# Optimization experiments

Hardware: AMD Instinct MI355X
Metric: run time of the kernel (lower is better)

Reference implementation:

```python
import jax, jax.numpy as jnp
import numpy as np

N = 5000
NFEAT = 512
NHID = 64
NHEADS = 8
NCLASS = 40
ALPHA = 0.2  # leaky relu slope
NEG_INF = -9e15


def setup_inputs() -> dict:
    key = jax.random.key(0)
    ks = jax.random.split(key, 12)
    x = jax.random.normal(ks[0], (N, NFEAT), dtype=jnp.float32)
    # binary adjacency, ~32 avg degree, with self loops
    adj = (jax.random.uniform(ks[1], (N, N)) < (32.0 / N)).astype(jnp.float32)
    adj = jnp.maximum(adj, jnp.eye(N, dtype=jnp.float32))
    s = 1.0 / np.sqrt(NFEAT)
    W_h = jax.random.uniform(ks[2], (NHEADS, NFEAT, NHID), minval=-s, maxval=s, dtype=jnp.float32)
    a_h = jax.random.uniform(ks[3], (NHEADS, 2 * NHID), minval=-s, maxval=s, dtype=jnp.float32)
    s2 = 1.0 / np.sqrt(NHID * NHEADS)
    W_o = jax.random.uniform(ks[4], (NHID * NHEADS, NHID), minval=-s2, maxval=s2, dtype=jnp.float32)
    a_o = jax.random.uniform(ks[5], (2 * NHID,), minval=-s2, maxval=s2, dtype=jnp.float32)
    s3 = 1.0 / np.sqrt(NHID)
    fc1_w = jax.random.uniform(ks[6], (NHID, 200), minval=-s3, maxval=s3, dtype=jnp.float32)
    fc1_b = jax.random.uniform(ks[7], (200,), minval=-s3, maxval=s3, dtype=jnp.float32)
    s4 = 1.0 / np.sqrt(200)
    fc2_w = jax.random.uniform(ks[8], (200, NCLASS), minval=-s4, maxval=s4, dtype=jnp.float32)
    fc2_b = jax.random.uniform(ks[9], (NCLASS,), minval=-s4, maxval=s4, dtype=jnp.float32)
    return {"x": x, "adj": adj, "W_h": W_h, "a_h": a_h, "W_o": W_o, "a_o": a_o,
            "fc1_w": fc1_w, "fc1_b": fc1_b, "fc2_w": fc2_w, "fc2_b": fc2_b}


def _masked_attention(e, adj):
    # e: [..., N, N]; mask where adj == 0, then row softmax
    e = jnp.where(adj > 0, e, NEG_INF)
    return jax.nn.softmax(e, axis=-1)


def reference(x, adj, W_h, a_h, W_o, a_o, fc1_w, fc1_b, fc2_w, fc2_b):
    # ---- multi-head GAT layer (concat=True), eval mode (dropout off) ----
    Wh = jnp.einsum('nf,hfo->hno', x, W_h)                 # [H, N, nhid]
    f1 = jnp.einsum('hno,ho->hn', Wh, a_h[:, :NHID])       # [H, N]
    f2 = jnp.einsum('hno,ho->hn', Wh, a_h[:, NHID:])       # [H, N]
    e = jax.nn.leaky_relu(f1[:, :, None] + f2[:, None, :], ALPHA)  # [H, N, N]
    att = _masked_attention(e, adj[None, :, :])
    h = jnp.einsum('hnm,hmo->hno', att, Wh)                # [H, N, nhid]
    h1 = jax.nn.elu(h).transpose(1, 0, 2).reshape(N, NHEADS * NHID)  # concat heads

    # ---- output GAT layer (concat=False) ----
    Wh2 = h1 @ W_o                                         # [N, nhid]
    g1 = Wh2 @ a_o[:NHID]                                  # [N]
    g2 = Wh2 @ a_o[NHID:]                                  # [N]
    e2 = jax.nn.leaky_relu(g1[:, None] + g2[None, :], ALPHA)
    att2 = _masked_attention(e2, adj)
    h2 = att2 @ Wh2                                        # [N, nhid]

    # ---- MLP head ----
    h3 = jax.nn.elu(h2 @ fc1_w + fc1_b)
    return h3 @ fc2_w + fc2_b                              # [N, nclass]
```

## Files before the change

kernel.cpp:

```cpp
#include <hip/hip_runtime.h>

typedef unsigned short u16;
typedef unsigned int u32;
typedef unsigned long long u64;
typedef __bf16 bf16_t;
typedef __bf16 bf16x8 __attribute__((ext_vector_type(8)));
typedef float f32x4 __attribute__((ext_vector_type(4)));
typedef u32 u32x4 __attribute__((ext_vector_type(4)));

#define NN 5000
#define NF 512
#define NH 64
#define HEADS 8
#define NCLS 40
#define CAP 128
#define LRELU 0.2f
#define BMW 80

#define CVT_BIG 320
#define CVT_GRID (CVT_BIG + 8)
#define BM_BLKS 1250
#define G1_BLKS (79 * HEADS)

__device__ __forceinline__ bool adj_is_bf16(const void* adj) {
    return ((*(const u32*)adj) & 0xFFFFu) != 0u;
}
__device__ __forceinline__ u16 rne_bf16(float f) {
    u32 u = __float_as_uint(f);
    u += 0x7FFFu + ((u >> 16) & 1u);
    return (u16)(u >> 16);
}
__device__ __forceinline__ float up_bf16(u16 h) {
    return __uint_as_float((u32)h << 16);
}
__device__ __forceinline__ u32x4 ntload4(const void* p, int idx) {
    return __builtin_nontemporal_load(((const u32x4*)p) + idx);
}

__global__ __launch_bounds__(256) void cvt(const void* __restrict__ x, const void* __restrict__ W_h,
                                           const void* __restrict__ adj,
                                           const void* a_h, const void* W_o, const void* a_o,
                                           const void* f1w, const void* f1b,
                                           const void* f2w, const void* f2b,
                                           u16* __restrict__ xc, u16* __restrict__ whc,
                                           float* a_hc, float* W_oc, float* a_oc,
                                           float* f1wc, float* f1bc, float* f2wc, float* f2bc) {
    const bool isb = adj_is_bf16(adj);
    const int b = blockIdx.x;
    if (b < CVT_BIG) {
        const int X4 = NN * NF / 4;
        const int T4 = X4 + HEADS * NF * NH / 4;
        for (int i = b * 256 + threadIdx.x; i < T4; i += CVT_BIG * 256) {
            if (i < X4) {
                ushort4 o;
                if (isb) {
                    o = ((const ushort4*)x)[i];
                } else {
                    u32x4 vv = ntload4(x, i);
                    o.x = rne_bf16(__uint_as_float(vv[0])); o.y = rne_bf16(__uint_as_float(vv[1]));
                    o.z = rne_bf16(__uint_as_float(vv[2])); o.w = rne_bf16(__uint_as_float(vv[3]));
                }
                ((ushort4*)xc)[i] = o;
            } else {
                const int iw = i - X4;
                u16 q[4];
                if (isb) {
                    ushort4 vv = ((const ushort4*)W_h)[iw];
                    q[0] = vv.x; q[1] = vv.y; q[2] = vv.z; q[3] = vv.w;
                } else {
                    u32x4 vv = ntload4(W_h, iw);
                    q[0] = rne_bf16(__uint_as_float(vv[0])); q[1] = rne_bf16(__uint_as_float(vv[1]));
                    q[2] = rne_bf16(__uint_as_float(vv[2])); q[3] = rne_bf16(__uint_as_float(vv[3]));
                }
                const int e0 = iw * 4;
                const int h = e0 >> 15;
                const int rem = e0 & 32767;
                const int f = rem >> 6, o0 = rem & 63;
                const int base = (h * 16 + (f >> 5)) * 2048 + ((f >> 3) & 3) * 128 + (f & 7);
                #pragma unroll
                for (int k = 0; k < 4; ++k) {
                    const int o = o0 + k;
                    whc[base + (o >> 4) * 512 + (o & 15) * 8] = q[k];
                }
            }
        }
    } else {
        const int s0 = HEADS * 2 * NH, s1 = HEADS * NH * NH, s2 = 2 * NH,
                  s3 = NH * 200, s4 = 200, s5 = 200 * NCLS, s6 = NCLS;
        const int total = s0 + s1 + s2 + s3 + s4 + s5 + s6;
        for (int i = (b - CVT_BIG) * 256 + threadIdx.x; i < total; i += 8 * 256) {
            const void* src; float* dst; int off = i;
            if (off < s0) { src = a_h; dst = a_hc; }
            else if ((off -= s0) < s1) { src = W_o;  dst = W_oc; }
            else if ((off -= s1) < s2) { src = a_o;  dst = a_oc; }
            else if ((off -= s2) < s3) { src = f1w;  dst = f1wc; }
            else if ((off -= s3) < s4) { src = f1b;  dst = f1bc; }
            else if ((off -= s4) < s5) { src = f2w;  dst = f2wc; }
            else { off -= s5;           src = f2b;  dst = f2bc; }
            dst[off] = isb ? up_bf16(((const u16*)src)[off]) : ((const float*)src)[off];
        }
    }
}

__global__ __launch_bounds__(256) void gemm1_f(const bf16_t* __restrict__ x,
                                               const bf16_t* __restrict__ Wf,
                                               const float* __restrict__ a_h,
                                               const void* __restrict__ adj,
                                               u64* __restrict__ bm,
                                               float* __restrict__ Wh,
                                               float* __restrict__ f1,
                                               float* __restrict__ f2) {
    const int lane = threadIdx.x & 63;
    const int wid  = threadIdx.x >> 6;
    const int b = blockIdx.x;

    if (b >= G1_BLKS) {
        const bool isb = adj_is_bf16(adj);
        const int r = (b - G1_BLKS) * 4 + wid;
        u64* bmrow = bm + (size_t)r * BMW;
        if (!isb) {
            const float* row = (const float*)adj + (size_t)r * NN;
            #pragma unroll
            for (int pass = 0; pass < 2; ++pass) {
                u32x4 v[10];
                #pragma unroll
                for (int k = 0; k < 10; ++k) {
                    int c = (pass * 10 + k) * 64 + lane;
                    v[k] = (c < 1250) ? ntload4(row, c) : (u32x4){0u, 0u, 0u, 0u};
                }
                #pragma unroll
                for (int k = 0; k < 10; ++k) {
                    int i = pass * 10 + k;
                    #pragma unroll
                    for (int j = 0; j < 4; ++j) {
                        u64 m = __ballot(v[k][j] != 0u);
                        if (lane == j) bmrow[i * 4 + j] = m;
                    }
                }
            }
        } else {
            const u16* row = (const u16*)adj + (size_t)r * NN;
            u32x4 v[10];
            #pragma unroll
            for (int k = 0; k < 10; ++k) {
                int c = k * 64 + lane;
                v[k] = (c < 625) ? ntload4(row, c) : (u32x4){0u, 0u, 0u, 0u};
            }
            #pragma unroll
            for (int k = 0; k < 10; ++k) {
                #pragma unroll
                for (int j = 0; j < 4; ++j) {
                    u64 mlo = __ballot((v[k][j] & 0xFFFFu) != 0u);
                    u64 mhi = __ballot((v[k][j] >> 16) != 0u);
                    if (lane == 2 * j)     bmrow[k * 8 + 2 * j]     = mlo;
                    if (lane == 2 * j + 1) bmrow[k * 8 + 2 * j + 1] = mhi;
                }
            }
        }
        return;
    }

    const int rg = b % 79;
    const int h  = b / 79;
    const int quad = lane >> 4;
    const int lr   = lane & 15;
    const int kq   = quad * 8;
    const int nCol = wid * 16 + lr;
    __shared__ float f1s[4][64], f2s[4][64];

    const bf16_t* Bf = Wf + (size_t)h * (16 * 2048) + threadIdx.x * 8;
    bf16x8 bfrag[16];
    #pragma unroll
    for (int s = 0; s < 16; ++s) bfrag[s] = *(const bf16x8*)(Bf + s * 2048);

    const float a1c = a_h[h * 128 + nCol];
    const float a2c = a_h[h * 128 + NH + nCol];

    for (int t = 0; t < 4; ++t) {
        const int rb = rg * 64 + t * 16;
        int row  = rb + lr;
        int rowc = row < NN ? row : NN - 1;
        const bf16_t* xp = x + (size_t)rowc * NF + kq;
        f32x4 acc = {0.f, 0.f, 0.f, 0.f};
        #pragma unroll
        for (int s = 0; s < 16; ++s) {
            bf16x8 a = *(const bf16x8*)(xp + s * 32);
            acc = __builtin_amdgcn_mfma_f32_16x16x32_bf16(a, bfrag[s], acc, 0, 0, 0);
        }
        #pragma unroll
        for (int r = 0; r < 4; ++r) {
            int gr = rb + quad * 4 + r;
            if (gr < NN) Wh[(size_t)gr * (HEADS * NH) + h * NH + nCol] = acc[r];
            float p1 = acc[r] * a1c, p2 = acc[r] * a2c;
            #pragma unroll
            for (int o = 8; o; o >>= 1) { p1 += __shfl_xor(p1, o); p2 += __shfl_xor(p2, o); }
            if (lr == 0) { f1s[wid][t * 16 + quad * 4 + r] = p1; f2s[wid][t * 16 + quad * 4 + r] = p2; }
        }
    }
    __syncthreads();
    if (wid == 0) {
        int gr = rg * 64 + lane;
        if (gr < NN) {
            f1[h * NN + gr] = f1s[0][lane] + f1s[1][lane] + f1s[2][lane] + f1s[3][lane];
            f2[h * NN + gr] = f2s[0][lane] + f2s[1][lane] + f2s[2][lane] + f2s[3][lane];
        }
    }
}

__global__ __launch_bounds__(256) void agg1f(const void* __restrict__ adj,
                                             const u64* __restrict__ bm,
                                             const float* __restrict__ Wh,
                                             const float* __restrict__ f1,
                                             const float* __restrict__ f2,
                                             int* __restrict__ nbr, int* __restrict__ deg,
                                             float* __restrict__ h1) {
    const bool isb = adj_is_bf16(adj);
    const int lane = threadIdx.x & 63;
    const int wid  = threadIdx.x >> 6;
    const int n = blockIdx.x;
    __shared__ int s_nbr[CAP];
    __shared__ int s_dall;
    __shared__ float s_p0[4][CAP], s_p1[4][CAP];

    if (wid == 0) {
        const u64* bmrow = bm + (size_t)n * BMW;
        int base = 0;
        #pragma unroll
        for (int r2 = 0; r2 < 2; ++r2) {
            int w = r2 * 64 + lane;
            u64 mw = (w < BMW) ? bmrow[w] : 0ull;
            int pc = __popcll(mw);
            int scan = pc;
            #pragma unroll
            for (int o = 1; o < 64; o <<= 1) {
                int t = __shfl_up(scan, o);
                if (lane >= o) scan += t;
            }
            int off = base + scan - pc;
            while (mw) {
                int bb = __ffsll(mw) - 1;
                mw &= mw - 1;
                int elem;
                if (!isb) elem = ((w >> 2) * 64 + bb) * 4 + (w & 3);
                else      elem = ((w >> 3) * 64 + bb) * 8 + (w & 7);
                if (off < CAP) s_nbr[off] = elem;
                ++off;
            }
            base += __shfl(scan, 63);
        }
        if (lane == 0) s_dall = base < CAP ? base : CAP;
    }
    __syncthreads();
    const int dall = s_dall;
    for (int i = threadIdx.x; i < dall; i += 256) nbr[(size_t)n * CAP + i] = s_nbr[i];
    if (threadIdx.x == 0) deg[n] = dall;

    const int ha = wid, hb = wid + 4;
    const int nb0 = (lane < dall) ? s_nbr[lane] : 0;
    const int nb1 = (lane + 64 < dall) ? s_nbr[lane + 64] : 0;
    const float f10 = f1[ha * NN + n], f11 = f1[hb * NN + n];
    const float* f2ha = f2 + (size_t)ha * NN;
    const float* f2hb = f2 + (size_t)hb * NN;

    float e00 = -INFINITY, e01 = -INFINITY, e10 = -INFINITY, e11 = -INFINITY;
    if (lane < dall) {
        float a = f10 + f2ha[nb0]; e00 = a > 0.f ? a : LRELU * a;
        float b = f11 + f2hb[nb0]; e10 = b > 0.f ? b : LRELU * b;
    }
    if (lane + 64 < dall) {
        float a = f10 + f2ha[nb1]; e01 = a > 0.f ? a : LRELU * a;
        float b = f11 + f2hb[nb1]; e11 = b > 0.f ? b : LRELU * b;
    }
    float mx0 = fmaxf(e00, e01), mx1 = fmaxf(e10, e11);
    #pragma unroll
    for (int o = 32; o; o >>= 1) {
        mx0 = fmaxf(mx0, __shfl_xor(mx0, o));
        mx1 = fmaxf(mx1, __shfl_xor(mx1, o));
    }
    float p00 = lane < dall ? expf(e00 - mx0) : 0.f;
    float p01 = lane + 64 < dall ? expf(e01 - mx0) : 0.f;
    float p10 = lane < dall ? expf(e10 - mx1) : 0.f;
    float p11 = lane + 64 < dall ? expf(e11 - mx1) : 0.f;
    float sm0 = p00 + p01, sm1 = p10 + p11;
    #pragma unroll
    for (int o = 32; o; o >>= 1) { sm0 += __shfl_xor(sm0, o); sm1 += __shfl_xor(sm1, o); }

    const float i0 = 1.f / sm0, i1 = 1.f / sm1;
    s_p0[wid][lane] = p00 * i0; s_p0[wid][lane + 64] = p01 * i0;
    s_p1[wid][lane] = p10 * i1; s_p1[wid][lane + 64] = p11 * i1;

    float A0 = 0.f, A1 = 0.f, A2 = 0.f, A3 = 0.f;
    float B0 = 0.f, B1 = 0.f, B2 = 0.f, B3 = 0.f;
    const float* W0 = Wh + ha * NH + lane;
    const float* W1 = Wh + hb * NH + lane;
    int j = 0;
    for (; j + 8 <= dall; j += 8) {
        #pragma unroll
        for (int u = 0; u < 8; ++u) {
            float a0 = s_p0[wid][j + u];
            float a1 = s_p1[wid][j + u];
            size_t base = (size_t)s_nbr[j + u] * (HEADS * NH);
            float w0 = W0[base], w1 = W1[base];
            if ((u & 3) == 0)      { A0 += a0 * w0; B0 += a1 * w1; }
            else if ((u & 3) == 1) { A1 += a0 * w0; B1 += a1 * w1; }
            else if ((u & 3) == 2) { A2 += a0 * w0; B2 += a1 * w1; }
            else                   { A3 += a0 * w0; B3 += a1 * w1; }
        }
    }
    for (; j < dall; ++j) {
        float a0 = s_p0[wid][j], a1 = s_p1[wid][j];
        size_t base = (size_t)s_nbr[j] * (HEADS * NH);
        A0 += a0 * W0[base]; B0 += a1 * W1[base];
    }
    float hv0 = A0 + A1 + A2 + A3;
    float hv1 = B0 + B1 + B2 + B3;
    hv0 = hv0 > 0.f ? hv0 : expf(hv0) - 1.f;
    hv1 = hv1 > 0.f ? hv1 : expf(hv1) - 1.f;
    h1[(size_t)n * (HEADS * NH) + ha * NH + lane] = hv0;
    h1[(size_t)n * (HEADS * NH) + hb * NH + lane] = hv1;
}

__global__ __launch_bounds__(256) void gemm2_4(const float* __restrict__ h1,
                                               const float* __restrict__ W_o,
                                               const float* __restrict__ a_o,
                                               float* __restrict__ Wh2,
                                               float* __restrict__ g1,
                                               float* __restrict__ g2) {
    const int t = threadIdx.x;
    const int n0 = blockIdx.x * 4;
    __shared__ float sh[4 * 512];
    __shared__ float ps[4][4][64];
    const float4* src = (const float4*)(h1 + (size_t)n0 * 512);
    ((float4*)sh)[t]       = src[t];
    ((float4*)sh)[t + 256] = src[t + 256];
    __syncthreads();
    const int o = t & 63, part = t >> 6;
    float a0 = 0.f, a1 = 0.f, a2 = 0.f, a3 = 0.f;
    const float* wo = W_o + part * 128 * 64 + o;
    const float* s0 = sh + part * 128;
    #pragma unroll 4
    for (int f = 0; f < 128; ++f) {
        float w = wo[f * 64];
        a0 += s0[f] * w; a1 += s0[512 + f] * w; a2 += s0[1024 + f] * w; a3 += s0[1536 + f] * w;
    }
    ps[part][0][o] = a0; ps[part][1][o] = a1; ps[part][2][o] = a2; ps[part][3][o] = a3;
    __syncthreads();
    const int nd = t >> 6;
    float w2 = ps[0][nd][o] + ps[1][nd][o] + ps[2][nd][o] + ps[3][nd][o];
    Wh2[(size_t)(n0 + nd) * 64 + o] = w2;
    float p1 = w2 * a_o[o], p2 = w2 * a_o[64 + o];
    #pragma unroll
    for (int s = 32; s; s >>= 1) { p1 += __shfl_xor(p1, s); p2 += __shfl_xor(p2, s); }
    if (o == 0) { g1[n0 + nd] = p1; g2[n0 + nd] = p2; }
}

__global__ __launch_bounds__(256) void agg2_mlp(const float* __restrict__ Wh2,
                                                const float* __restrict__ g1,
                                                const float* __restrict__ g2,
                                                const int* __restrict__ nbr,
                                                const int* __restrict__ deg,
                                                const float* __restrict__ fc1_w,
                                                const float* __restrict__ fc1_b,
                                                const float* __restrict__ fc2_w,
                                                const float* __restrict__ fc2_b,
                                                float* __restrict__ out) {
    const int lane = threadIdx.x & 63;
    const int wid  = threadIdx.x >> 6;
    const int t = threadIdx.x;
    const int n0 = blockIdx.x * 4;
    const int n = n0 + wid;
    __shared__ float s_alpha[4][CAP];
    __shared__ int   s_nbr[4][CAP];
    __shared__ float s_h2[4][NH];
    __shared__ float s_h3[4][200];
    __shared__ float ps2[2][4][NCLS];
    const int d = deg[n];
    const int* nb = nbr + (size_t)n * CAP;
    const float gn = g1[n];

    float mx = -INFINITY;
    for (int j = lane; j < d; j += 64) {
        int m = nb[j];
        s_nbr[wid][j] = m;
        float e = gn + g2[m];
        e = e > 0.f ? e : LRELU * e;
        s_alpha[wid][j] = e;
        mx = fmaxf(mx, e);
    }
    #pragma unroll
    for (int o = 32; o; o >>= 1) mx = fmaxf(mx, __shfl_xor(mx, o));
    float sm = 0.f;
    for (int j = lane; j < d; j += 64) {
        float p = expf(s_alpha[wid][j] - mx);
        s_alpha[wid][j] = p;
        sm += p;
    }
    #pragma unroll
    for (int o = 32; o; o >>= 1) sm += __shfl_xor(sm, o);

    float acc0 = 0.f, acc1 = 0.f, acc2 = 0.f, acc3 = 0.f;
    int j = 0;
    for (; j + 4 <= d; j += 4) {
        acc0 += s_alpha[wid][j]     * Wh2[(size_t)s_nbr[wid][j]     * NH + lane];
        acc1 += s_alpha[wid][j + 1] * Wh2[(size_t)s_nbr[wid][j + 1] * NH + lane];
        acc2 += s_alpha[wid][j + 2] * Wh2[(size_t)s_nbr[wid][j + 2] * NH + lane];
        acc3 += s_alpha[wid][j + 3] * Wh2[(size_t)s_nbr[wid][j + 3] * NH + lane];
    }
    for (; j < d; ++j) acc0 += s_alpha[wid][j] * Wh2[(size_t)s_nbr[wid][j] * NH + lane];
    s_h2[wid][lane] = (acc0 + acc1 + acc2 + acc3) / sm;
    __syncthreads();

    if (t < 200) {
        float b0 = 0.f, b1 = 0.f, b2 = 0.f, b3 = 0.f;
        #pragma unroll 4
        for (int f = 0; f < NH; ++f) {
            float w = fc1_w[f * 200 + t];
            b0 += s_h2[0][f] * w; b1 += s_h2[1][f] * w; b2 += s_h2[2][f] * w; b3 += s_h2[3][f] * w;
        }
        float bb = fc1_b[t];
        b0 += bb; b1 += bb; b2 += bb; b3 += bb;
        s_h3[0][t] = b0 > 0.f ? b0 : expf(b0) - 1.f;
        s_h3[1][t] = b1 > 0.f ? b1 : expf(b1) - 1.f;
        s_h3[2][t] = b2 > 0.f ? b2 : expf(b2) - 1.f;
        s_h3[3][t] = b3 > 0.f ? b3 : expf(b3) - 1.f;
    }
    __syncthreads();

    if (t < 80) {
        const int o = t % 40, fh = t / 40;
        float c0 = 0.f, c1 = 0.f, c2 = 0.f, c3 = 0.f;
        #pragma unroll 4
        for (int f = fh * 100; f < fh * 100 + 100; ++f) {
            float w = fc2_w[f * NCLS + o];
            c0 += s_h3[0][f] * w; c1 += s_h3[1][f] * w; c2 += s_h3[2][f] * w; c3 += s_h3[3][f] * w;
        }
        ps2[fh][0][o] = c0; ps2[fh][1][o] = c1; ps2[fh][2][o] = c2; ps2[fh][3][o] = c3;
    }
    __syncthreads();
    if (t < 160) {
        const int nd = t / 40, o = t % 40;
        out[(size_t)(n0 + nd) * NCLS + o] = ps2[0][nd][o] + ps2[1][nd][o] + fc2_b[o];
    }
}

extern "C" void kernel_launch(void* const* d_in, const int* in_sizes, int n_in,
                              void* d_out, int out_size, void* d_ws, size_t ws_size,
                              hipStream_t stream) {
    const void* x     = d_in[0];
    const void* adj   = d_in[1];
    const void* W_h   = d_in[2];
    const void* a_h   = d_in[3];
    const void* W_o   = d_in[4];
    const void* a_o   = d_in[5];
    const void* fc1_w = d_in[6];
    const void* fc1_b = d_in[7];
    const void* fc2_w = d_in[8];
    const void* fc2_b = d_in[9];
    float* out = (float*)d_out;

    char* ws = (char*)d_ws;
    int*   nbr   = (int*)(ws + 0);
    int*   deg   = (int*)(ws + 2560000);
    float* Wh    = (float*)(ws + 2580000);
    float* f1    = (float*)(ws + 12820000);
    float* f2    = (float*)(ws + 12980000);
    float* h1    = (float*)(ws + 13140000);
    float* Wh2   = (float*)(ws + 23380000);
    float* g1    = (float*)(ws + 24660000);
    float* g2    = (float*)(ws + 24680000);
    u16*   xc    = (u16*)(ws + 24700000);
    u16*   whc   = (u16*)(ws + 29820000);
    float* a_hc  = (float*)(ws + 30344288);
    float* W_oc  = (float*)(ws + 30348384);
    float* a_oc  = (float*)(ws + 30479456);
    float* f1wc  = (float*)(ws + 30479968);
    float* f1bc  = (float*)(ws + 30531168);
    float* f2wc  = (float*)(ws + 30531968);
    float* f2bc  = (float*)(ws + 30563968);
    u64*   bm    = (u64*)(ws + 30564128);

    cvt<<<CVT_GRID, 256, 0, stream>>>(x, W_h, adj, a_h, W_o, a_o,
                                      fc1_w, fc1_b, fc2_w, fc2_b,
                                      xc, whc, a_hc, W_oc, a_oc,
                                      f1wc, f1bc, f2wc, f2bc);
    gemm1_f<<<G1_BLKS + BM_BLKS, 256, 0, stream>>>((const bf16_t*)xc, (const bf16_t*)whc,
                                                   a_hc, adj, bm, Wh, f1, f2);
    agg1f<<<NN, 256, 0, stream>>>(adj, bm, Wh, f1, f2, nbr, deg, h1);
    gemm2_4<<<NN / 4, 256, 0, stream>>>(h1, W_oc, a_oc, Wh2, g1, g2);
    agg2_mlp<<<NN / 4, 256, 0, stream>>>(Wh2, g1, g2, nbr, deg,
                                         f1wc, f1bc, f2wc, f2bc, out);
}
```

Baseline: 271.6 us.

## Build neighbor lists in adjacency scan and vectorize attention aggregation

The adjacency scan in the gemm1 kernel now compacts its ballot masks straight into per-row neighbor index lists and degrees. This drops the intermediate bitmask buffer and the serial compaction that one wave of every agg1f block used to do. agg1f now just loads the precomputed neighbor list, writes all eight heads' attention weights to shared memory, and has each lane gather float2 pairs across two heads for coalesced 128-column reads. The costs are an extra block-wide barrier and more serial ffs work in the scan blocks.

After: 268.9 us. About the same (-1.0%).

```diff
diff --git a/kernel.cpp b/kernel.cpp
--- a/kernel.cpp
+++ b/kernel.cpp
@@ -15,7 +15,6 @@
 #define NCLS 40
 #define CAP 128
 #define LRELU 0.2f
-#define BMW 80
 
 #define CVT_BIG 320
 #define CVT_GRID (CVT_BIG + 8)
@@ -106,7 +105,7 @@
                                                const bf16_t* __restrict__ Wf,
                                                const float* __restrict__ a_h,
                                                const void* __restrict__ adj,
-                                               u64* __restrict__ bm,
+                                               int* __restrict__ nbr, int* __restrict__ deg,
                                                float* __restrict__ Wh,
                                                float* __restrict__ f1,
                                                float* __restrict__ f2) {
@@ -117,7 +116,7 @@
     if (b >= G1_BLKS) {
         const bool isb = adj_is_bf16(adj);
         const int r = (b - G1_BLKS) * 4 + wid;
-        u64* bmrow = bm + (size_t)r * BMW;
+        u64 my0 = 0ull, my1 = 0ull;
         if (!isb) {
             const float* row = (const float*)adj + (size_t)r * NN;
             #pragma unroll
@@ -134,7 +133,9 @@
                     #pragma unroll
                     for (int j = 0; j < 4; ++j) {
                         u64 m = __ballot(v[k][j] != 0u);
-                        if (lane == j) bmrow[i * 4 + j] = m;
+                        int w = i * 4 + j;
+                        if (w == lane)      my0 = m;
+                        if (w == lane + 64) my1 = m;
                     }
                 }
             }
@@ -152,11 +153,58 @@
                 for (int j = 0; j < 4; ++j) {
                     u64 mlo = __ballot((v[k][j] & 0xFFFFu) != 0u);
                     u64 mhi = __ballot((v[k][j] >> 16) != 0u);
-                    if (lane == 2 * j)     bmrow[k * 8 + 2 * j]     = mlo;
-                    if (lane == 2 * j + 1) bmrow[k * 8 + 2 * j + 1] = mhi;
+                    int wl = k * 8 + 2 * j, wh = wl + 1;
+                    if (wl == lane)      my0 = mlo;
+                    if (wl == lane + 64) my1 = mlo;
+                    if (wh == lane)      my0 = mhi;
+                    if (wh == lane + 64) my1 = mhi;
                 }
             }
         }
+        int* nrow = nbr + (size_t)r * CAP;
+        int pc = __popcll(my0);
+        int scan = pc;
+        #pragma unroll
+        for (int o = 1; o < 64; o <<= 1) {
+            int t2 = __shfl_up(scan, o);
+            if (lane >= o) scan += t2;
+        }
+        int off = scan - pc;
+        {
+            const int w = lane;
+            u64 mw = my0;
+            while (mw) {
+                int bb = __ffsll(mw) - 1;
+                mw &= mw - 1;
+                int elem = !isb ? ((w >> 2) * 64 + bb) * 4 + (w & 3)
+                                : ((w >> 3) * 64 + bb) * 8 + (w & 7);
+                if (off < CAP) nrow[off] = elem;
+                ++off;
+            }
+        }
+        const int base = __shfl(scan, 63);
+        int pc1 = __popcll(my1);
+        int scan1 = pc1;
+        #pragma unroll
+        for (int o = 1; o < 64; o <<= 1) {
+            int t2 = __shfl_up(scan1, o);
+            if (lane >= o) scan1 += t2;
+        }
+        int off1 = base + scan1 - pc1;
+        {
+            const int w = lane + 64;
+            u64 mw = my1;
+            while (mw) {
+                int bb = __ffsll(mw) - 1;
+                mw &= mw - 1;
+                int elem = !isb ? ((w >> 2) * 64 + bb) * 4 + (w & 3)
+                                : ((w >> 3) * 64 + bb) * 8 + (w & 7);
+                if (off1 < CAP) nrow[off1] = elem;
+                ++off1;
+            }
+        }
+        const int total = base + __shfl(scan1, 63);
+        if (lane == 0) deg[r] = total < CAP ? total : CAP;
         return;
     }
 
@@ -207,67 +255,34 @@
     }
 }
 
-__global__ __launch_bounds__(256) void agg1f(const void* __restrict__ adj,
-                                             const u64* __restrict__ bm,
+__global__ __launch_bounds__(256) void agg1f(const int* __restrict__ nbr,
+                                             const int* __restrict__ deg,
                                              const float* __restrict__ Wh,
                                              const float* __restrict__ f1,
                                              const float* __restrict__ f2,
-                                             int* __restrict__ nbr, int* __restrict__ deg,
                                              float* __restrict__ h1) {
-    const bool isb = adj_is_bf16(adj);
     const int lane = threadIdx.x & 63;
     const int wid  = threadIdx.x >> 6;
     const int n = blockIdx.x;
     __shared__ int s_nbr[CAP];
-    __shared__ int s_dall;
-    __shared__ float s_p0[4][CAP], s_p1[4][CAP];
-
-    if (wid == 0) {
-        const u64* bmrow = bm + (size_t)n * BMW;
-        int base = 0;
-        #pragma unroll
-        for (int r2 = 0; r2 < 2; ++r2) {
-            int w = r2 * 64 + lane;
-            u64 mw = (w < BMW) ? bmrow[w] : 0ull;
-            int pc = __popcll(mw);
-            int scan = pc;
-            #pragma unroll
-            for (int o = 1; o < 64; o <<= 1) {
-                int t = __shfl_up(scan, o);
-                if (lane >= o) scan += t;
-            }
-            int off = base + scan - pc;
-            while (mw) {
-                int bb = __ffsll(mw) - 1;
-                mw &= mw - 1;
-                int elem;
-                if (!isb) elem = ((w >> 2) * 64 + bb) * 4 + (w & 3);
-                else      elem = ((w >> 3) * 64 + bb) * 8 + (w & 7);
-                if (off < CAP) s_nbr[off] = elem;
-                ++off;
-            }
-            base += __shfl(scan, 63);
-        }
-        if (lane == 0) s_dall = base < CAP ? base : CAP;
-    }
-    __syncthreads();
-    const int dall = s_dall;
-    for (int i = threadIdx.x; i < dall; i += 256) nbr[(size_t)n * CAP + i] = s_nbr[i];
-    if (threadIdx.x == 0) deg[n] = dall;
+    __shared__ float s_p[8][CAP];
+    const int d = deg[n];
+    for (int i = threadIdx.x; i < d; i += 256) s_nbr[i] = nbr[(size_t)n * CAP + i];
+    __syncthreads();
 
     const int ha = wid, hb = wid + 4;
-    const int nb0 = (lane < dall) ? s_nbr[lane] : 0;
-    const int nb1 = (lane + 64 < dall) ? s_nbr[lane + 64] : 0;
+    const int nb0 = (lane < d) ? s_nbr[lane] : 0;
+    const int nb1 = (lane + 64 < d) ? s_nbr[lane + 64] : 0;
     const float f10 = f1[ha * NN + n], f11 = f1[hb * NN + n];
     const float* f2ha = f2 + (size_t)ha * NN;
     const float* f2hb = f2 + (size_t)hb * NN;
 
     float e00 = -INFINITY, e01 = -INFINITY, e10 = -INFINITY, e11 = -INFINITY;
-    if (lane < dall) {
+    if (lane < d) {
         float a = f10 + f2ha[nb0]; e00 = a > 0.f ? a : LRELU * a;
         float b = f11 + f2hb[nb0]; e10 = b > 0.f ? b : LRELU * b;
     }
-    if (lane + 64 < dall) {
+    if (lane + 64 < d) {
         float a = f10 + f2ha[nb1]; e01 = a > 0.f ? a : LRELU * a;
         float b = f11 + f2hb[nb1]; e11 = b > 0.f ? b : LRELU * b;
     }
@@ -277,47 +292,45 @@
         mx0 = fmaxf(mx0, __shfl_xor(mx0, o));
         mx1 = fmaxf(mx1, __shfl_xor(mx1, o));
     }
-    float p00 = lane < dall ? expf(e00 - mx0) : 0.f;
-    float p01 = lane + 64 < dall ? expf(e01 - mx0) : 0.f;
-    float p10 = lane < dall ? expf(e10 - mx1) : 0.f;
-    float p11 = lane + 64 < dall ? expf(e11 - mx1) : 0.f;
+    float p00 = lane < d ? expf(e00 - mx0) : 0.f;
+    float p01 = lane + 64 < d ? expf(e01 - mx0) : 0.f;
+    float p10 = lane < d ? expf(e10 - mx1) : 0.f;
+    float p11 = lane + 64 < d ? expf(e11 - mx1) : 0.f;
     float sm0 = p00 + p01, sm1 = p10 + p11;
     #pragma unroll
     for (int o = 32; o; o >>= 1) { sm0 += __shfl_xor(sm0, o); sm1 += __shfl_xor(sm1, o); }
 
     const float i0 = 1.f / sm0, i1 = 1.f / sm1;
-    s_p0[wid][lane] = p00 * i0; s_p0[wid][lane + 64] = p01 * i0;
-    s_p1[wid][lane] = p10 * i1; s_p1[wid][lane + 64] = p11 * i1;
-
-    float A0 = 0.f, A1 = 0.f, A2 = 0.f, A3 = 0.f;
-    float B0 = 0.f, B1 = 0.f, B2 = 0.f, B3 = 0.f;
-    const float* W0 = Wh + ha * NH + lane;
-    const float* W1 = Wh + hb * NH + lane;
+    s_p[ha][lane] = p00 * i0; s_p[ha][lane + 64] = p01 * i0;
+    s_p[hb][lane] = p10 * i1; s_p[hb][lane + 64] = p11 * i1;
+    __syncthreads();
+
+    const float* ap = s_p[2 * wid + (lane >> 5)];
+    const float* wp = Wh + wid * 128 + 2 * lane;
+    float A0x = 0.f, A0y = 0.f, A1x = 0.f, A1y = 0.f;
+    float A2x = 0.f, A2y = 0.f, A3x = 0.f, A3y = 0.f;
     int j = 0;
-    for (; j + 8 <= dall; j += 8) {
+    for (; j + 8 <= d; j += 8) {
         #pragma unroll
         for (int u = 0; u < 8; ++u) {
-            float a0 = s_p0[wid][j + u];
-            float a1 = s_p1[wid][j + u];
-            size_t base = (size_t)s_nbr[j + u] * (HEADS * NH);
-            float w0 = W0[base], w1 = W1[base];
-            if ((u & 3) == 0)      { A0 += a0 * w0; B0 += a1 * w1; }
-            else if ((u & 3) == 1) { A1 += a0 * w0; B1 += a1 * w1; }
-            else if ((u & 3) == 2) { A2 += a0 * w0; B2 += a1 * w1; }
-            else                   { A3 += a0 * w0; B3 += a1 * w1; }
-        }
-    }
-    for (; j < dall; ++j) {
-        float a0 = s_p0[wid][j], a1 = s_p1[wid][j];
-        size_t base = (size_t)s_nbr[j] * (HEADS * NH);
-        A0 += a0 * W0[base]; B0 += a1 * W1[base];
-    }
-    float hv0 = A0 + A1 + A2 + A3;
-    float hv1 = B0 + B1 + B2 + B3;
-    hv0 = hv0 > 0.f ? hv0 : expf(hv0) - 1.f;
-    hv1 = hv1 > 0.f ? hv1 : expf(hv1) - 1.f;
-    h1[(size_t)n * (HEADS * NH) + ha * NH + lane] = hv0;
-    h1[(size_t)n * (HEADS * NH) + hb * NH + lane] = hv1;
+            const float2 v = *(const float2*)(wp + (size_t)s_nbr[j + u] * (HEADS * NH));
+            const float a = ap[j + u];
+            if ((u & 3) == 0)      { A0x += a * v.x; A0y += a * v.y; }
+            else if ((u & 3) == 1) { A1x += a * v.x; A1y += a * v.y; }
+            else if ((u & 3) == 2) { A2x += a * v.x; A2y += a * v.y; }
+            else                   { A3x += a * v.x; A3y += a * v.y; }
+        }
+    }
+    for (; j < d; ++j) {
+        const float2 v = *(const float2*)(wp + (size_t)s_nbr[j] * (HEADS * NH));
+        const float a = ap[j];
+        A0x += a * v.x; A0y += a * v.y;
+    }
+    float hx = A0x + A1x + A2x + A3x;
+    float hy = A0y + A1y + A2y + A3y;
+    hx = hx > 0.f ? hx : expf(hx) - 1.f;
+    hy = hy > 0.f ? hy : expf(hy) - 1.f;
+    *(float2*)(h1 + (size_t)n * (HEADS * NH) + wid * 128 + 2 * lane) = make_float2(hx, hy);
 }
 
 __global__ __launch_bounds__(256) void gemm2_4(const float* __restrict__ h1,
@@ -477,15 +490,14 @@
     float* f1bc  = (float*)(ws + 30531168);
     float* f2wc  = (float*)(ws + 30531968);
     float* f2bc  = (float*)(ws + 30563968);
-    u64*   bm    = (u64*)(ws + 30564128);
 
     cvt<<<CVT_GRID, 256, 0, stream>>>(x, W_h, adj, a_h, W_o, a_o,
                                       fc1_w, fc1_b, fc2_w, fc2_b,
                                       xc, whc, a_hc, W_oc, a_oc,
                                       f1wc, f1bc, f2wc, f2bc);
     gemm1_f<<<G1_BLKS + BM_BLKS, 256, 0, stream>>>((const bf16_t*)xc, (const bf16_t*)whc,
-                                                   a_hc, adj, bm, Wh, f1, f2);
-    agg1f<<<NN, 256, 0, stream>>>(adj, bm, Wh, f1, f2, nbr, deg, h1);
+                                                   a_hc, adj, nbr, deg, Wh, f1, f2);
+    agg1f<<<NN, 256, 0, stream>>>(nbr, deg, Wh, f1, f2, h1);
     gemm2_4<<<NN / 4, 256, 0, stream>>>(h1, W_oc, a_oc, Wh2, g1, g2);
     agg2_mlp<<<NN / 4, 256, 0, stream>>>(Wh2, g1, g2, nbr, deg,
                                          f1wc, f1bc, f2wc, f2bc, out);
```
